# Kernel optimization log

Hardware: AMD Instinct MI355X
Metric: run time of the kernel (lower is better)

Reference implementation:

```python
import jax, jax.numpy as jnp
import numpy as np

# Static config (matches init_kwargs / chosen geometry)
DIM, HEADS, WS, SHIFT = 96, 3, 7, 3
H, W = 56, 56
B = 64
N = WS * WS
HID = int(DIM * 4.0)
EPS = 1e-5


def _rel_tables():
    # relative_coords_table: (1, 2*WS-1, 2*WS-1, 2), log-spaced coords in [-1,1]
    c = np.arange(-(WS - 1), WS, dtype=np.float32)
    tab = np.stack(np.meshgrid(c, c, indexing='ij'), axis=-1)[None]
    tab = tab / (WS - 1) * 8.0
    tab = np.sign(tab) * np.log2(np.abs(tab) + 1.0) / np.log2(8.0)
    # relative_position_index: (N, N) int
    coords = np.stack(np.meshgrid(np.arange(WS), np.arange(WS), indexing='ij'))
    cf = coords.reshape(2, -1)
    rel = (cf[:, :, None] - cf[:, None, :]).transpose(1, 2, 0).astype(np.int64)
    rel[..., 0] += WS - 1
    rel[..., 1] += WS - 1
    rel[..., 0] *= 2 * WS - 1
    return jnp.asarray(tab), jnp.asarray(rel.sum(-1))

_TABLE, _RPI = _rel_tables()


def _shift_mask():
    # standard SW-MSA mask: (num_windows, N, N), 0 / -100
    img = np.zeros((1, H, W, 1), dtype=np.float32)
    cnt = 0
    segs = (slice(0, -WS), slice(-WS, -SHIFT), slice(-SHIFT, None))
    for hs in segs:
        for ws_ in segs:
            img[:, hs, ws_, :] = cnt
            cnt += 1
    mw = img.reshape(1, H // WS, WS, W // WS, WS, 1).transpose(0, 1, 3, 2, 4, 5).reshape(-1, N)
    am = mw[:, None, :] - mw[:, :, None]
    return jnp.asarray(np.where(am != 0, -100.0, 0.0).astype(np.float32))


def _ln(x, g, b):
    mu = x.mean(-1, keepdims=True)
    var = x.var(-1, keepdims=True)
    return (x - mu) * jax.lax.rsqrt(var + EPS) * g + b


def setup_inputs() -> dict:
    key = jax.random.key(0)
    ks = jax.random.split(key, 8)
    s = 0.02
    return {
        'x': jax.random.normal(ks[0], (B, H * W, DIM), jnp.float32),
        'attn_mask': _shift_mask(),
        'qkv_w': jax.random.normal(ks[1], (3 * DIM, DIM), jnp.float32) * s,
        'q_bias': jnp.zeros((DIM,), jnp.float32),
        'v_bias': jnp.zeros((DIM,), jnp.float32),
        'logit_scale': jnp.full((HEADS, 1, 1), np.log(10.0), jnp.float32),
        'cpb_w1': jax.random.normal(ks[2], (512, 2), jnp.float32) * s,
        'cpb_b1': jnp.zeros((512,), jnp.float32),
        'cpb_w2': jax.random.normal(ks[3], (HEADS, 512), jnp.float32) * s,
        'proj_w': jax.random.normal(ks[4], (DIM, DIM), jnp.float32) * s,
        'proj_b': jnp.zeros((DIM,), jnp.float32),
        'norm1_g': jnp.ones((DIM,), jnp.float32),
        'norm1_b': jnp.zeros((DIM,), jnp.float32),
        'fc1_w': jax.random.normal(ks[5], (HID, DIM), jnp.float32) * s,
        'fc1_b': jnp.zeros((HID,), jnp.float32),
        'fc2_w': jax.random.normal(ks[6], (DIM, HID), jnp.float32) * s,
        'fc2_b': jnp.zeros((DIM,), jnp.float32),
        'norm2_g': jnp.ones((DIM,), jnp.float32),
        'norm2_b': jnp.zeros((DIM,), jnp.float32),
    }


def reference(x, attn_mask, qkv_w, q_bias, v_bias, logit_scale, cpb_w1, cpb_b1,
              cpb_w2, proj_w, proj_b, norm1_g, norm1_b, fc1_w, fc1_b, fc2_w,
              fc2_b, norm2_g, norm2_b):
    Bx, L, C = x.shape
    d = C // HEADS
    nH, nWd = H // WS, W // WS
    shortcut = x

    xi = x.reshape(Bx, H, W, C)
    xi = jnp.roll(xi, (-SHIFT, -SHIFT), axis=(1, 2))
    # window partition -> (Bx*nH*nWd, N, C)
    xw = xi.reshape(Bx, nH, WS, nWd, WS, C).transpose(0, 1, 3, 2, 4, 5).reshape(-1, N, C)

    # qkv with q/v bias only (k bias fixed to zero)
    qkv_bias = jnp.concatenate([q_bias, jnp.zeros_like(v_bias), v_bias])
    qkv = (xw @ qkv_w.T + qkv_bias).reshape(-1, N, 3, HEADS, d).transpose(2, 0, 3, 1, 4)
    q, k, v = qkv[0], qkv[1], qkv[2]  # (B_, h, N, d)

    # cosine attention with clamped learnable temperature
    qn = q / jnp.maximum(jnp.linalg.norm(q, axis=-1, keepdims=True), 1e-12)
    kn = k / jnp.maximum(jnp.linalg.norm(k, axis=-1, keepdims=True), 1e-12)
    attn = jnp.einsum('bhnd,bhmd->bhnm', qn, kn)
    scale = jnp.exp(jnp.minimum(logit_scale, jnp.log(jnp.float32(100.0))))
    attn = attn * scale

    # continuous relative position bias via cpb_mlp
    tab = jax.nn.gelu(_TABLE @ cpb_w1.T + cpb_b1, approximate=False) @ cpb_w2.T
    tab = tab.reshape(-1, HEADS)
    rpb = tab[_RPI.reshape(-1)].reshape(N, N, HEADS).transpose(2, 0, 1)
    attn = attn + (16.0 * jax.nn.sigmoid(rpb))[None]

    # shift mask
    nWin = attn_mask.shape[0]
    attn = attn.reshape(-1, nWin, HEADS, N, N) + attn_mask[None, :, None]
    attn = jax.nn.softmax(attn.reshape(-1, HEADS, N, N), axis=-1)

    out = jnp.einsum('bhnm,bhmd->bnhd', attn, v).reshape(-1, N, C)
    out = out @ proj_w.T + proj_b

    # window reverse + un-shift
    out = out.reshape(Bx, nH, nWd, WS, WS, C).transpose(0, 1, 3, 2, 4, 5).reshape(Bx, H, W, C)
    out = jnp.roll(out, (SHIFT, SHIFT), axis=(1, 2)).reshape(Bx, L, C)

    # SwinV2 post-norm residuals
    x1 = shortcut + _ln(out, norm1_g, norm1_b)
    h = jax.nn.gelu(x1 @ fc1_w.T + fc1_b, approximate=False) @ fc2_w.T + fc2_b
    return x1 + _ln(h, norm2_g, norm2_b)
```

## Files before the change

kernel.cpp:

```cpp
#include <hip/hip_runtime.h>
#include <math.h>

#define BATCH 64
#define HW 56
#define CDIM 96
#define NHEADS 3
#define WSZ 7
#define NTOK 49
#define SHIFT_ 3
#define NWIN_TOT 4096
#define HID 384
#define NTOKENS (BATCH * HW * HW)
#define LN100 4.6051702f

typedef __attribute__((ext_vector_type(8))) short bf16x8;
typedef __attribute__((ext_vector_type(8))) _Float16 f16x8;
typedef __attribute__((ext_vector_type(4))) float f32x4;

__device__ inline f32x4 mfma16(bf16x8 a, bf16x8 b, f32x4 c) {
  return __builtin_amdgcn_mfma_f32_16x16x32_bf16(a, b, c, 0, 0, 0);
}
__device__ inline f32x4 mfma16h(f16x8 a, f16x8 b, f32x4 c) {
  return __builtin_amdgcn_mfma_f32_16x16x32_f16(a, b, c, 0, 0, 0);
}

__device__ inline unsigned short f2b(float f) {
  unsigned u = __float_as_uint(f);
  unsigned r = (u + 0x7FFFu + ((u >> 16) & 1u)) >> 16;
  return (unsigned short)r;
}
__device__ inline float blo(unsigned u) { return __uint_as_float(u << 16); }
__device__ inline float bhi(unsigned u) { return __uint_as_float(u & 0xFFFF0000u); }
__device__ inline unsigned packb(float a, float b) {
  return (unsigned)f2b(a) | ((unsigned)f2b(b) << 16);
}
__device__ inline unsigned packh(float a, float b) {
  _Float16 ha = (_Float16)a, hb = (_Float16)b;
  unsigned short ua = *(unsigned short*)&ha, ub = *(unsigned short*)&hb;
  return (unsigned)ua | ((unsigned)ub << 16);
}
__device__ inline float gelu_f(float v) {
  float a = fabsf(v) * 0.70710678118654752f;
  float t = 1.0f / fmaf(a, 0.3275911f, 1.0f);
  float p = t * fmaf(t, fmaf(t, fmaf(t, fmaf(t, 1.061405429f, -1.453152027f),
                                     1.421413741f), -0.284496736f), 0.254829592f);
  float er = 1.0f - p * __expf(-a * a);
  er = (v < 0.f) ? -er : er;
  return 0.5f * v * (1.0f + er);
}

__global__ __launch_bounds__(256) void wconv2_kernel(
    const float* __restrict__ qkv_w, const float* __restrict__ fc1_w,
    const float* __restrict__ fc2_w, const float* __restrict__ proj_w,
    unsigned* __restrict__ qkvf, unsigned* __restrict__ w1f,
    unsigned* __restrict__ w2f, unsigned* __restrict__ pwf) {
  int T = blockIdx.x * 256 + threadIdx.x;
  if (T < 3456) {
    int tk = T >> 6, l = T & 63;
    int n = tk / 3, ks = tk - n * 3;
    int o = n * 16 + (l & 15);
    const float* src = qkv_w + o * 96 + ks * 32 + (l >> 4) * 8;
    uint4 d;
    d.x = packb(src[0], src[1]); d.y = packb(src[2], src[3]);
    d.z = packb(src[4], src[5]); d.w = packb(src[6], src[7]);
    *(uint4*)&qkvf[(size_t)(tk * 64 + l) * 4] = d;
    return;
  }
  T -= 3456;
  if (T < 4608) {
    int tk = T >> 6, l = T & 63;
    int n = tk / 3, ks = tk - n * 3;
    int o = n * 16 + (l & 15);
    const float* src = fc1_w + o * 96 + ks * 32 + (l >> 4) * 8;
    uint4 d;
    d.x = packb(src[0], src[1]); d.y = packb(src[2], src[3]);
    d.z = packb(src[4], src[5]); d.w = packb(src[6], src[7]);
    *(uint4*)&w1f[(size_t)(tk * 64 + l) * 4] = d;
    return;
  }
  T -= 4608;
  if (T < 4608) {
    int tk = T >> 6, l = T & 63;
    int n = tk / 12, ks = tk - n * 12;
    int o = n * 16 + (l & 15);
    const float* src = fc2_w + o * 384 + ks * 32 + (l >> 4) * 8;
    uint4 d;
    d.x = packb(src[0], src[1]); d.y = packb(src[2], src[3]);
    d.z = packb(src[4], src[5]); d.w = packb(src[6], src[7]);
    *(uint4*)&w2f[(size_t)(tk * 64 + l) * 4] = d;
    return;
  }
  T -= 4608;
  if (T < 1152) {
    int tk = T >> 6, l = T & 63;
    int n = tk / 3, ks = tk - n * 3;
    int o = n * 16 + (l & 15);
    const float* src = proj_w + o * 96 + ks * 32 + (l >> 4) * 8;
    uint4 d;
    d.x = packb(src[0], src[1]); d.y = packb(src[2], src[3]);
    d.z = packb(src[4], src[5]); d.w = packb(src[6], src[7]);
    *(uint4*)&pwf[(size_t)(tk * 64 + l) * 4] = d;
  }
}

__global__ __launch_bounds__(512) void cpb_table_kernel(
    const float* __restrict__ w1, const float* __restrict__ b1,
    const float* __restrict__ w2, float* __restrict__ tabout) {
  int tid = threadIdx.x;
  if (tid >= 169 * 3) return;
  int e = tid / 3, h = tid - e * 3;
  int i = e / 13, j = e - i * 13;
  float ti = (float)(i - 6) * (8.0f / 6.0f);
  float tj = (float)(j - 6) * (8.0f / 6.0f);
  float sx = (ti > 0.f) ? 1.f : (ti < 0.f ? -1.f : 0.f);
  float sy = (tj > 0.f) ? 1.f : (tj < 0.f ? -1.f : 0.f);
  float tx = sx * log2f(fabsf(ti) + 1.f) * (1.0f / 3.0f);
  float ty = sy * log2f(fabsf(tj) + 1.f) * (1.0f / 3.0f);
  float acc = 0.f;
  for (int jj = 0; jj < 512; ++jj) {
    float hv = tx * w1[jj * 2 + 0] + ty * w1[jj * 2 + 1] + b1[jj];
    float g = 0.5f * hv * (1.f + erff(hv * 0.70710678118654752f));
    acc += g * w2[h * 512 + jj];
  }
  tabout[e * 3 + h] = acc;
}

__global__ __launch_bounds__(256) void bias_kernel(
    const float* __restrict__ tabout, float* __restrict__ bias16) {
  int idx = blockIdx.x * 256 + threadIdx.x;
  if (idx >= NHEADS * NTOK * NTOK) return;
  int h = idx / (NTOK * NTOK);
  int rem = idx - h * NTOK * NTOK;
  int i = rem / NTOK, j = rem - i * NTOK;
  int ri = (i / WSZ) - (j / WSZ) + 6;
  int ci = (i % WSZ) - (j % WSZ) + 6;
  int e = ri * 13 + ci;
  float v = tabout[e * 3 + h];
  bias16[idx] = 16.f / (1.f + expf(-v));
}

__global__ __launch_bounds__(256) void qkv_mfma_kernel(
    const float* __restrict__ x, const unsigned* __restrict__ qkvf,
    const float* __restrict__ q_bias, const float* __restrict__ v_bias,
    const float* __restrict__ logit_scale,
    unsigned* __restrict__ qws, unsigned* __restrict__ kws,
    unsigned* __restrict__ vws) {
  __shared__ unsigned xa[64 * 52];
  int tid = threadIdx.x, lane = tid & 63, wv = tid >> 6;
  size_t tok0 = (size_t)blockIdx.x * 64;

  for (int idx = tid; idx < 3072; idx += 256) {
    int t = idx / 48, c2 = idx - t * 48;
    const float2 s = *(const float2*)(x + (tok0 + t) * 96 + c2 * 2);
    xa[t * 52 + c2] = packb(s.x, s.y);
  }
  __syncthreads();

  int c15 = lane & 15, q4 = lane >> 4;
  bf16x8 afr[3];
  #pragma unroll
  for (int k = 0; k < 3; ++k)
    afr[k] = *(const bf16x8*)&xa[(wv * 16 + c15) * 52 + k * 16 + q4 * 4];

  f32x4 acc[18];
  #pragma unroll
  for (int n = 0; n < 18; ++n) acc[n] = f32x4{0.f, 0.f, 0.f, 0.f};
  #pragma unroll
  for (int n = 0; n < 18; ++n) {
    #pragma unroll
    for (int k = 0; k < 3; ++k) {
      bf16x8 b = *(const bf16x8*)&qkvf[(size_t)((n * 3 + k) * 64 + lane) * 4];
      acc[n] = mfma16(afr[k], b, acc[n]);
    }
  }

  int tokr0 = (int)tok0 + wv * 16 + q4 * 4;
  #pragma unroll
  for (int h = 0; h < 3; ++h) {
    float sc = expf(fminf(logit_scale[h], LN100));
    {
      f32x4 a0 = acc[2 * h], a1 = acc[2 * h + 1];
      float b0 = q_bias[h * 32 + c15], b1 = q_bias[h * 32 + 16 + c15];
      unsigned pk[8];
      #pragma unroll
      for (int i = 0; i < 4; ++i) {
        float va = a0[i] + b0, vb = a1[i] + b1;
        float ss = va * va + vb * vb;
        ss += __shfl_xor(ss, 1, 64); ss += __shfl_xor(ss, 2, 64);
        ss += __shfl_xor(ss, 4, 64); ss += __shfl_xor(ss, 8, 64);
        float inv = sc / fmaxf(sqrtf(ss), 1e-12f);
        va *= inv; vb *= inv;
        float pa = __shfl_xor(va, 1, 64), pb = __shfl_xor(vb, 1, 64);
        pk[i] = packb(va, pa); pk[4 + i] = packb(vb, pb);
      }
      if (!(lane & 1)) {
        int dw0 = c15 >> 1;
        #pragma unroll
        for (int i = 0; i < 4; ++i) {
          size_t base = ((size_t)(tokr0 + i) * 3 + h) * 16;
          qws[base + dw0] = pk[i];
          qws[base + 8 + dw0] = pk[4 + i];
        }
      }
    }
    {
      f32x4 a0 = acc[6 + 2 * h], a1 = acc[7 + 2 * h];
      unsigned pk[8];
      #pragma unroll
      for (int i = 0; i < 4; ++i) {
        float va = a0[i], vb = a1[i];
        float ss = va * va + vb * vb;
        ss += __shfl_xor(ss, 1, 64); ss += __shfl_xor(ss, 2, 64);
        ss += __shfl_xor(ss, 4, 64); ss += __shfl_xor(ss, 8, 64);
        float inv = 1.f / fmaxf(sqrtf(ss), 1e-12f);
        va *= inv; vb *= inv;
        float pa = __shfl_xor(va, 1, 64), pb = __shfl_xor(vb, 1, 64);
        pk[i] = packb(va, pa); pk[4 + i] = packb(vb, pb);
      }
      if (!(lane & 1)) {
        int dw0 = c15 >> 1;
        #pragma unroll
        for (int i = 0; i < 4; ++i) {
          size_t base = ((size_t)(tokr0 + i) * 3 + h) * 16;
          kws[base + dw0] = pk[i];
          kws[base + 8 + dw0] = pk[4 + i];
        }
      }
    }
    {
      f32x4 a0 = acc[12 + 2 * h], a1 = acc[13 + 2 * h];
      float b0 = v_bias[h * 32 + c15], b1 = v_bias[h * 32 + 16 + c15];
      unsigned pk[8];
      #pragma unroll
      for (int i = 0; i < 4; ++i) {
        float va = a0[i] + b0, vb = a1[i] + b1;
        float pa = __shfl_xor(va, 1, 64), pb = __shfl_xor(vb, 1, 64);
        pk[i] = packb(va, pa); pk[4 + i] = packb(vb, pb);
      }
      if (!(lane & 1)) {
        int dw0 = c15 >> 1;
        #pragma unroll
        for (int i = 0; i < 4; ++i) {
          size_t base = ((size_t)(tokr0 + i) * 3 + h) * 16;
          vws[base + dw0] = pk[i];
          vws[base + 8 + dw0] = pk[4 + i];
        }
      }
    }
  }
}

__global__ __launch_bounds__(256) void attn_fused_kernel(
    const unsigned* __restrict__ qws, const unsigned* __restrict__ kws,
    const unsigned* __restrict__ vws, const float* __restrict__ bias16,
    const float* __restrict__ mask, const unsigned* __restrict__ pwf,
    const float* __restrict__ proj_b, const float* __restrict__ x,
    const float* __restrict__ n1g, const float* __restrict__ n1b,
    float* __restrict__ out) {
  __shared__ __align__(16) unsigned smem[10432];
  _Float16* VtS  = (_Float16*)smem;
  unsigned* obuf = (unsigned*)smem;
  _Float16* Ph   = (_Float16*)((char*)smem + 13824);
  unsigned* Phd  = (unsigned*)((char*)smem + 13824);
  float*    ybuf = (float*)((char*)smem + 13824);
  int*      toks = (int*)((char*)smem + 41472);

  int tid = threadIdx.x, lane = tid & 63, wv = tid >> 6;
  int c15 = lane & 15, q4 = lane >> 4;
  int win = blockIdx.x;
  int b = win >> 6, wi = win & 63, wh = wi >> 3, wcx = wi & 7;

  if (tid < 64) {
    int t = tid < 49 ? tid : 48;
    int tr = (t * 9363) >> 16, tc = t - tr * 7;
    int R = wh * 7 + tr + SHIFT_; if (R >= HW) R -= HW;
    int C = wcx * 7 + tc + SHIFT_; if (C >= HW) C -= HW;
    toks[tid] = b * 3136 + R * 56 + C;
  }
  __syncthreads();

  bf16x8 qf[4], kf[4];
  if (wv < 3) {
    #pragma unroll
    for (int m = 0; m < 4; ++m)
      qf[m] = *(const bf16x8*)&qws[((size_t)toks[m * 16 + c15] * 3 + wv) * 16 + q4 * 4];
    #pragma unroll
    for (int n = 0; n < 4; ++n)
      kf[n] = *(const bf16x8*)&kws[((size_t)toks[n * 16 + c15] * 3 + wv) * 16 + q4 * 4];
  }

  for (int idx = tid; idx < 768; idx += 256) {
    int h2 = idx >> 8, rem = idx & 255;
    int t = rem >> 2, dg = rem & 3;
    uint4 v4 = *(const uint4*)&vws[((size_t)toks[t] * 3 + h2) * 16 + dg * 4];
    _Float16* dst = &VtS[h2 * 2304 + (dg * 8) * 72 + t];
    dst[0 * 72] = (_Float16)blo(v4.x); dst[1 * 72] = (_Float16)bhi(v4.x);
    dst[2 * 72] = (_Float16)blo(v4.y); dst[3 * 72] = (_Float16)bhi(v4.y);
    dst[4 * 72] = (_Float16)blo(v4.z); dst[5 * 72] = (_Float16)bhi(v4.z);
    dst[6 * 72] = (_Float16)blo(v4.w); dst[7 * 72] = (_Float16)bhi(v4.w);
  }
  __syncthreads();

  f32x4 o[4][2];
  #pragma unroll
  for (int m = 0; m < 4; ++m)
    #pragma unroll
    for (int n2 = 0; n2 < 2; ++n2) o[m][n2] = f32x4{0.f, 0.f, 0.f, 0.f};

  if (wv < 3) {
    int h = wv;
    f32x4 s[4][4];
    #pragma unroll
    for (int m = 0; m < 4; ++m)
      #pragma unroll
      for (int n = 0; n < 4; ++n)
        s[m][n] = mfma16(qf[m], kf[n], f32x4{0.f, 0.f, 0.f, 0.f});

    const float* bsl = bias16 + h * 2401;
    const float* msl = mask + (size_t)wi * 2401;
    #pragma unroll
    for (int m = 0; m < 4; ++m) {
      #pragma unroll
      for (int i = 0; i < 4; ++i) {
        int rw = m * 16 + 4 * q4 + i;
        if (rw < 49) {
          const float* br = bsl + rw * 49;
          const float* mr = msl + rw * 49;
          #pragma unroll
          for (int n = 0; n < 4; ++n) {
            int j = n * 16 + c15;
            s[m][n][i] = (j < 49) ? (s[m][n][i] + br[j] + mr[j]) : -1e30f;
          }
        } else {
          #pragma unroll
          for (int n = 0; n < 4; ++n)
            if (n * 16 + c15 >= 49) s[m][n][i] = -1e30f;
        }
      }
    }

    #pragma unroll
    for (int m = 0; m < 4; ++m) {
      #pragma unroll
      for (int i = 0; i < 4; ++i) {
        float mx = fmaxf(fmaxf(s[m][0][i], s[m][1][i]), fmaxf(s[m][2][i], s[m][3][i]));
        mx = fmaxf(mx, __shfl_xor(mx, 1, 64)); mx = fmaxf(mx, __shfl_xor(mx, 2, 64));
        mx = fmaxf(mx, __shfl_xor(mx, 4, 64)); mx = fmaxf(mx, __shfl_xor(mx, 8, 64));
        float sum = 0.f;
        #pragma unroll
        for (int n = 0; n < 4; ++n) { float e = __expf(s[m][n][i] - mx); s[m][n][i] = e; sum += e; }
        sum += __shfl_xor(sum, 1, 64); sum += __shfl_xor(sum, 2, 64);
        sum += __shfl_xor(sum, 4, 64); sum += __shfl_xor(sum, 8, 64);
        float inv = 1.f / sum;
        #pragma unroll
        for (int n = 0; n < 4; ++n) s[m][n][i] *= inv;
      }
    }

    #pragma unroll
    for (int m = 0; m < 4; ++m)
      #pragma unroll
      for (int n = 0; n < 4; ++n)
        #pragma unroll
        for (int i = 0; i < 4; ++i) {
          float pv = s[m][n][i];
          float pn = __shfl_xor(pv, 1, 64);
          if (!(lane & 1)) {
            int row = m * 16 + 4 * q4 + i;
            Phd[h * 2304 + row * 36 + n * 8 + (c15 >> 1)] = packh(pv, pn);
          }
        }
    asm volatile("s_waitcnt lgkmcnt(0)" ::: "memory");
    __builtin_amdgcn_sched_barrier(0);

    #pragma unroll
    for (int ks = 0; ks < 2; ++ks) {
      f16x8 pa[4];
      #pragma unroll
      for (int m = 0; m < 4; ++m)
        pa[m] = *(const f16x8*)&Ph[h * 4608 + (m * 16 + c15) * 72 + ks * 32 + q4 * 8];
      #pragma unroll
      for (int n2 = 0; n2 < 2; ++n2) {
        f16x8 vb = *(const f16x8*)&VtS[h * 2304 + (n2 * 16 + c15) * 72 + ks * 32 + q4 * 8];
        #pragma unroll
        for (int m = 0; m < 4; ++m) o[m][n2] = mfma16h(pa[m], vb, o[m][n2]);
      }
    }
  }
  __syncthreads();

  if (wv < 3) {
    int h = wv;
    #pragma unroll
    for (int m = 0; m < 4; ++m)
      #pragma unroll
      for (int n2 = 0; n2 < 2; ++n2)
        #pragma unroll
        for (int i = 0; i < 4; ++i) {
          float ov = o[m][n2][i];
          float on = __shfl_xor(ov, 1, 64);
          if (!(lane & 1))
            obuf[(m * 16 + 4 * q4 + i) * 52 + h * 16 + n2 * 8 + (c15 >> 1)] = packb(ov, on);
        }
  }
  __syncthreads();

  bf16x8 oa[3];
  #pragma unroll
  for (int ks = 0; ks < 3; ++ks)
    oa[ks] = *(const bf16x8*)&obuf[(wv * 16 + c15) * 52 + ks * 16 + q4 * 4];
  f32x4 pr[6];
  #pragma unroll
  for (int n = 0; n < 6; ++n) pr[n] = f32x4{0.f, 0.f, 0.f, 0.f};
  #pragma unroll
  for (int n = 0; n < 6; ++n)
    #pragma unroll
    for (int ks = 0; ks < 3; ++ks) {
      bf16x8 bfr = *(const bf16x8*)&pwf[(size_t)((n * 3 + ks) * 64 + lane) * 4];
      pr[n] = mfma16(oa[ks], bfr, pr[n]);
    }

  #pragma unroll
  for (int n = 0; n < 6; ++n) {
    int col = n * 16 + c15;
    float bo = proj_b[col];
    #pragma unroll
    for (int i = 0; i < 4; ++i)
      ybuf[(wv * 16 + 4 * q4 + i) * 100 + col] = pr[n][i] + bo;
  }
  __syncthreads();

  int t = tid >> 2, pp = tid & 3;
  if (t < 49) {
    const float* yrow = ybuf + t * 100 + pp * 24;
    float s1 = 0.f;
    #pragma unroll
    for (int c = 0; c < 24; ++c) s1 += yrow[c];
    s1 += __shfl_xor(s1, 1, 64); s1 += __shfl_xor(s1, 2, 64);
    float mu = s1 * (1.f / 96.f);
    float v2 = 0.f;
    #pragma unroll
    for (int c = 0; c < 24; ++c) { float d = yrow[c] - mu; v2 += d * d; }
    v2 += __shfl_xor(v2, 1, 64); v2 += __shfl_xor(v2, 2, 64);
    float rs = rsqrtf(v2 * (1.f / 96.f) + 1e-5f);
    size_t base = (size_t)toks[t] * 96 + pp * 24;
    #pragma unroll
    for (int c4 = 0; c4 < 6; ++c4) {
      float4 xv = *(const float4*)(x + base + c4 * 4);
      float4 gv = *(const float4*)(n1g + pp * 24 + c4 * 4);
      float4 bv = *(const float4*)(n1b + pp * 24 + c4 * 4);
      float4 ov;
      ov.x = xv.x + (yrow[c4 * 4 + 0] - mu) * rs * gv.x + bv.x;
      ov.y = xv.y + (yrow[c4 * 4 + 1] - mu) * rs * gv.y + bv.y;
      ov.z = xv.z + (yrow[c4 * 4 + 2] - mu) * rs * gv.z + bv.z;
      ov.w = xv.w + (yrow[c4 * 4 + 3] - mu) * rs * gv.w + bv.w;
      *(float4*)(out + base + c4 * 4) = ov;
    }
  }
}

__global__ __launch_bounds__(256) void mlp_mfma_kernel(
    const unsigned* __restrict__ w1f, const float* __restrict__ fc1_b,
    const unsigned* __restrict__ w2f, const float* __restrict__ fc2_b,
    const float* __restrict__ n2g, const float* __restrict__ n2b,
    float* __restrict__ xio) {
  __shared__ unsigned xa[64 * 52];
  __shared__ unsigned hid[64 * 196];
  __shared__ float mu_s[64], rs_s[64];
  int tid = threadIdx.x, lane = tid & 63, wv = tid >> 6;
  int c15 = lane & 15, q4 = lane >> 4;
  size_t tok0 = (size_t)blockIdx.x * 64;

  for (int idx = tid; idx < 3072; idx += 256) {
    int t = idx / 48, c2 = idx - t * 48;
    const float2 s = *(const float2*)(xio + (tok0 + t) * 96 + c2 * 2);
    xa[t * 52 + c2] = packb(s.x, s.y);
  }
  __syncthreads();

  bf16x8 afr[4][3];
  #pragma unroll
  for (int m = 0; m < 4; ++m)
    #pragma unroll
    for (int k = 0; k < 3; ++k)
      afr[m][k] = *(const bf16x8*)&xa[(m * 16 + c15) * 52 + k * 16 + q4 * 4];
  f32x4 acc[4][6];
  #pragma unroll
  for (int m = 0; m < 4; ++m)
    #pragma unroll
    for (int n = 0; n < 6; ++n) acc[m][n] = f32x4{0.f, 0.f, 0.f, 0.f};
  #pragma unroll
  for (int n = 0; n < 6; ++n) {
    #pragma unroll
    for (int k = 0; k < 3; ++k) {
      bf16x8 b = *(const bf16x8*)&w1f[(size_t)(((6 * wv + n) * 3 + k) * 64 + lane) * 4];
      #pragma unroll
      for (int m = 0; m < 4; ++m) acc[m][n] = mfma16(afr[m][k], b, acc[m][n]);
    }
  }
  unsigned short* hidb = (unsigned short*)hid;
  #pragma unroll
  for (int n = 0; n < 6; ++n) {
    int col = (6 * wv + n) * 16 + c15;
    float bo = fc1_b[col];
    #pragma unroll
    for (int m = 0; m < 4; ++m) {
      #pragma unroll
      for (int i = 0; i < 4; ++i) {
        float g = gelu_f(acc[m][n][i] + bo);
        hidb[(m * 16 + q4 * 4 + i) * 392 + col] = f2b(g);
      }
    }
  }
  __syncthreads();

  f32x4 acc2[6];
  #pragma unroll
  for (int n = 0; n < 6; ++n) acc2[n] = f32x4{0.f, 0.f, 0.f, 0.f};
  #pragma unroll
  for (int k = 0; k < 12; ++k) {
    bf16x8 a = *(const bf16x8*)&hid[(wv * 16 + c15) * 196 + k * 16 + q4 * 4];
    #pragma unroll
    for (int n = 0; n < 6; ++n) {
      bf16x8 b = *(const bf16x8*)&w2f[(size_t)((n * 12 + k) * 64 + lane) * 4];
      acc2[n] = mfma16(a, b, acc2[n]);
    }
  }
  __syncthreads();

  float* ybuf = (float*)hid;
  #pragma unroll
  for (int n = 0; n < 6; ++n) {
    int col = n * 16 + c15;
    float bo = fc2_b[col];
    #pragma unroll
    for (int i = 0; i < 4; ++i)
      ybuf[(wv * 16 + q4 * 4 + i) * 100 + col] = acc2[n][i] + bo;
  }
  __syncthreads();

  {
    int t = tid >> 2, p = tid & 3;
    const float* row = ybuf + t * 100 + p * 24;
    float s = 0.f, s2 = 0.f;
    for (int c = 0; c < 24; ++c) { float v = row[c]; s += v; s2 += v * v; }
    s += __shfl_xor(s, 1, 64); s2 += __shfl_xor(s2, 1, 64);
    s += __shfl_xor(s, 2, 64); s2 += __shfl_xor(s2, 2, 64);
    if (p == 0) {
      float mu = s * (1.f / 96.f);
      float var = s2 * (1.f / 96.f) - mu * mu;
      mu_s[t] = mu;
      rs_s[t] = rsqrtf(fmaxf(var, 0.f) + 1e-5f);
    }
  }
  __syncthreads();

  for (int idx = tid; idx < 1536; idx += 256) {
    int t = idx / 24, c4 = (idx - t * 24) * 4;
    float mu = mu_s[t], rs = rs_s[t];
    float4 y4 = *(float4*)&ybuf[t * 100 + c4];
    float4 g4 = *(const float4*)&n2g[c4];
    float4 b4 = *(const float4*)&n2b[c4];
    float* gp = &xio[tok0 * 96 + t * 96 + c4];
    float4 x4 = *(const float4*)gp;
    float4 ov;
    ov.x = x4.x + (y4.x - mu) * rs * g4.x + b4.x;
    ov.y = x4.y + (y4.y - mu) * rs * g4.y + b4.y;
    ov.z = x4.z + (y4.z - mu) * rs * g4.z + b4.z;
    ov.w = x4.w + (y4.w - mu) * rs * g4.w + b4.w;
    *(float4*)gp = ov;
  }
}

extern "C" void kernel_launch(void* const* d_in, const int* in_sizes, int n_in,
                              void* d_out, int out_size, void* d_ws, size_t ws_size,
                              hipStream_t stream) {
  const float* x           = (const float*)d_in[0];
  const float* attn_mask   = (const float*)d_in[1];
  const float* qkv_w       = (const float*)d_in[2];
  const float* q_bias      = (const float*)d_in[3];
  const float* v_bias      = (const float*)d_in[4];
  const float* logit_scale = (const float*)d_in[5];
  const float* cpb_w1      = (const float*)d_in[6];
  const float* cpb_b1      = (const float*)d_in[7];
  const float* cpb_w2      = (const float*)d_in[8];
  const float* proj_w      = (const float*)d_in[9];
  const float* proj_b      = (const float*)d_in[10];
  const float* n1g         = (const float*)d_in[11];
  const float* n1b         = (const float*)d_in[12];
  const float* fc1_w       = (const float*)d_in[13];
  const float* fc1_b       = (const float*)d_in[14];
  const float* fc2_w       = (const float*)d_in[15];
  const float* fc2_b       = (const float*)d_in[16];
  const float* n2g         = (const float*)d_in[17];
  const float* n2b         = (const float*)d_in[18];
  float* out = (float*)d_out;

  float* tab     = (float*)d_ws;
  float* bias16  = tab + 512;
  unsigned* qkvf = (unsigned*)(bias16 + 7296);
  unsigned* w1f  = qkvf + 13824;
  unsigned* w2f  = w1f + 18432;
  unsigned* pwf  = w2f + 18432;
  unsigned* qws  = pwf + 4608;
  unsigned* kws  = qws + 9633792;
  unsigned* vws  = kws + 9633792;

  wconv2_kernel<<<54, 256, 0, stream>>>(qkv_w, fc1_w, fc2_w, proj_w,
                                        qkvf, w1f, w2f, pwf);
  cpb_table_kernel<<<1, 512, 0, stream>>>(cpb_w1, cpb_b1, cpb_w2, tab);
  bias_kernel<<<(NHEADS * NTOK * NTOK + 255) / 256, 256, 0, stream>>>(tab, bias16);
  qkv_mfma_kernel<<<NTOKENS / 64, 256, 0, stream>>>(x, qkvf, q_bias, v_bias,
                                                    logit_scale, qws, kws, vws);
  attn_fused_kernel<<<NWIN_TOT, 256, 0, stream>>>(qws, kws, vws, bias16, attn_mask,
                                                  pwf, proj_b, x, n1g, n1b, out);
  mlp_mfma_kernel<<<NTOKENS / 64, 256, 0, stream>>>(w1f, fc1_b, w2f, fc2_b,
                                                    n2g, n2b, out);
}
```

Baseline: 498.1 us.

## Store QKV workspace in shifted-window-major layout to make attention loads contiguous

The QKV kernel now writes q/k/v into a workspace ordered by shifted window, head and token, computing each token's window index at write time. The attention kernel then reads its window's q, k and v from a contiguous region instead of gathering per-token rows through a shared-memory token table. This removes the token-table setup, one block barrier and the scattered gather reads. The cost is scattered writes and extra integer division in the QKV epilogue.

```diff
diff --git a/kernel.cpp b/kernel.cpp
--- a/kernel.cpp
+++ b/kernel.cpp
@@ -175,6 +175,19 @@
   }
 
   int tokr0 = (int)tok0 + wv * 16 + q4 * 4;
+  int wbase[4];
+  #pragma unroll
+  for (int i = 0; i < 4; ++i) {
+    int tk = tokr0 + i;
+    int bb = tk / 3136, rem = tk - bb * 3136;
+    int R = rem / 56, C = rem - R * 56;
+    int rr = R + 53; if (rr >= 56) rr -= 56;
+    int cc = C + 53; if (cc >= 56) cc -= 56;
+    int wr = rr / 7, tr2 = rr - wr * 7;
+    int wc = cc / 7, tc2 = cc - wc * 7;
+    wbase[i] = (bb * 64 + wr * 8 + wc) * 2352 + (tr2 * 7 + tc2) * 16;
+  }
+
   #pragma unroll
   for (int h = 0; h < 3; ++h) {
     float sc = expf(fminf(logit_scale[h], LN100));
@@ -197,7 +210,7 @@
         int dw0 = c15 >> 1;
         #pragma unroll
         for (int i = 0; i < 4; ++i) {
-          size_t base = ((size_t)(tokr0 + i) * 3 + h) * 16;
+          size_t base = (size_t)wbase[i] + h * 784;
           qws[base + dw0] = pk[i];
           qws[base + 8 + dw0] = pk[4 + i];
         }
@@ -221,7 +234,7 @@
         int dw0 = c15 >> 1;
         #pragma unroll
         for (int i = 0; i < 4; ++i) {
-          size_t base = ((size_t)(tokr0 + i) * 3 + h) * 16;
+          size_t base = (size_t)wbase[i] + h * 784;
           kws[base + dw0] = pk[i];
           kws[base + 8 + dw0] = pk[4 + i];
         }
@@ -241,7 +254,7 @@
         int dw0 = c15 >> 1;
         #pragma unroll
         for (int i = 0; i < 4; ++i) {
-          size_t base = ((size_t)(tokr0 + i) * 3 + h) * 16;
+          size_t base = (size_t)wbase[i] + h * 784;
           vws[base + dw0] = pk[i];
           vws[base + 8 + dw0] = pk[4 + i];
         }
@@ -257,42 +270,39 @@
     const float* __restrict__ proj_b, const float* __restrict__ x,
     const float* __restrict__ n1g, const float* __restrict__ n1b,
     float* __restrict__ out) {
-  __shared__ __align__(16) unsigned smem[10432];
+  __shared__ __align__(16) unsigned smem[10368];
   _Float16* VtS  = (_Float16*)smem;
   unsigned* obuf = (unsigned*)smem;
   _Float16* Ph   = (_Float16*)((char*)smem + 13824);
   unsigned* Phd  = (unsigned*)((char*)smem + 13824);
   float*    ybuf = (float*)((char*)smem + 13824);
-  int*      toks = (int*)((char*)smem + 41472);
 
   int tid = threadIdx.x, lane = tid & 63, wv = tid >> 6;
   int c15 = lane & 15, q4 = lane >> 4;
   int win = blockIdx.x;
   int b = win >> 6, wi = win & 63, wh = wi >> 3, wcx = wi & 7;
-
-  if (tid < 64) {
-    int t = tid < 49 ? tid : 48;
-    int tr = (t * 9363) >> 16, tc = t - tr * 7;
-    int R = wh * 7 + tr + SHIFT_; if (R >= HW) R -= HW;
-    int C = wcx * 7 + tc + SHIFT_; if (C >= HW) C -= HW;
-    toks[tid] = b * 3136 + R * 56 + C;
-  }
-  __syncthreads();
+  size_t wroot = (size_t)win * 2352;
 
   bf16x8 qf[4], kf[4];
   if (wv < 3) {
-    #pragma unroll
-    for (int m = 0; m < 4; ++m)
-      qf[m] = *(const bf16x8*)&qws[((size_t)toks[m * 16 + c15] * 3 + wv) * 16 + q4 * 4];
-    #pragma unroll
-    for (int n = 0; n < 4; ++n)
-      kf[n] = *(const bf16x8*)&kws[((size_t)toks[n * 16 + c15] * 3 + wv) * 16 + q4 * 4];
+    size_t wb = wroot + (size_t)wv * 784;
+    #pragma unroll
+    for (int m = 0; m < 4; ++m) {
+      int t = m * 16 + c15; if (t > 48) t = 48;
+      qf[m] = *(const bf16x8*)&qws[wb + t * 16 + q4 * 4];
+    }
+    #pragma unroll
+    for (int n = 0; n < 4; ++n) {
+      int t = n * 16 + c15; if (t > 48) t = 48;
+      kf[n] = *(const bf16x8*)&kws[wb + t * 16 + q4 * 4];
+    }
   }
 
   for (int idx = tid; idx < 768; idx += 256) {
     int h2 = idx >> 8, rem = idx & 255;
     int t = rem >> 2, dg = rem & 3;
-    uint4 v4 = *(const uint4*)&vws[((size_t)toks[t] * 3 + h2) * 16 + dg * 4];
+    int tc2 = t > 48 ? 48 : t;
+    uint4 v4 = *(const uint4*)&vws[wroot + h2 * 784 + tc2 * 16 + dg * 4];
     _Float16* dst = &VtS[h2 * 2304 + (dg * 8) * 72 + t];
     dst[0 * 72] = (_Float16)blo(v4.x); dst[1 * 72] = (_Float16)bhi(v4.x);
     dst[2 * 72] = (_Float16)blo(v4.y); dst[3 * 72] = (_Float16)bhi(v4.y);
@@ -443,7 +453,10 @@
     for (int c = 0; c < 24; ++c) { float d = yrow[c] - mu; v2 += d * d; }
     v2 += __shfl_xor(v2, 1, 64); v2 += __shfl_xor(v2, 2, 64);
     float rs = rsqrtf(v2 * (1.f / 96.f) + 1e-5f);
-    size_t base = (size_t)toks[t] * 96 + pp * 24;
+    int tr = (t * 9363) >> 16, tc = t - tr * 7;
+    int R = wh * 7 + tr + SHIFT_; if (R >= HW) R -= HW;
+    int C = wcx * 7 + tc + SHIFT_; if (C >= HW) C -= HW;
+    size_t base = ((size_t)(b * 3136 + R * 56 + C)) * 96 + pp * 24;
     #pragma unroll
     for (int c4 = 0; c4 < 6; ++c4) {
       float4 xv = *(const float4*)(x + base + c4 * 4);
```

After: 478.3 us. 1.04x faster.
